# Kernel tuning notes

Hardware: AMD Instinct MI355X
Metric: run time of the kernel (lower is better)

The kernel has to match this reference:

```python
import math
import jax, jax.numpy as jnp
import numpy as np

H = 1024        # hidden_size
V = 32000       # target vocab
T = 64          # decoder steps
B = 32          # batch
NL = 2          # lstm layers
WSZ = 50        # window_size
WLEN = 2 * WSZ + 1
L = 128         # source length (all sequences full)
S = L + WLEN    # padded encoder length, guarantees windows in-bounds
HH = math.ceil(H / 2)
STD2 = (WSZ / 2.0) ** 2
EPS = 1e-14


def setup_inputs():
    key = jax.random.key(0)
    ks = jax.random.split(key, 16)
    sc = 0.02
    inp = {}
    inp["encoder_output"] = jax.random.normal(ks[0], (S, B, H), jnp.float32)
    inp["context"] = jax.random.normal(ks[1], (T, B, H), jnp.float32)
    inp["h0"] = jax.random.normal(ks[2], (NL, B, H), jnp.float32)
    inp["c0"] = jax.random.normal(ks[3], (NL, B, H), jnp.float32)
    inp["embedding"] = jax.random.normal(ks[4], (V, H), jnp.float32) * sc
    inp["attn_w1"] = jax.random.normal(ks[5], (HH, H), jnp.float32) * sc
    inp["attn_b1"] = jnp.zeros((HH,), jnp.float32)
    inp["attn_w2"] = jax.random.normal(ks[6], (1, HH), jnp.float32) * sc
    inp["attn_b2"] = jnp.zeros((1,), jnp.float32)
    inp["lstm_Wih0"] = jax.random.normal(ks[7], (4 * H, 2 * H), jnp.float32) * sc  # input feeding: 2H input
    inp["lstm_Whh0"] = jax.random.normal(ks[8], (4 * H, H), jnp.float32) * sc
    inp["lstm_bih0"] = jnp.zeros((4 * H,), jnp.float32)
    inp["lstm_bhh0"] = jnp.zeros((4 * H,), jnp.float32)
    inp["lstm_Wih1"] = jax.random.normal(ks[9], (4 * H, H), jnp.float32) * sc
    inp["lstm_Whh1"] = jax.random.normal(ks[10], (4 * H, H), jnp.float32) * sc
    inp["lstm_bih1"] = jnp.zeros((4 * H,), jnp.float32)
    inp["lstm_bhh1"] = jnp.zeros((4 * H,), jnp.float32)
    inp["fc1_w"] = jax.random.normal(ks[11], (H, 2 * H), jnp.float32) * sc
    inp["fc1_b"] = jnp.zeros((H,), jnp.float32)
    inp["fc2_w"] = jax.random.normal(ks[12], (V, H), jnp.float32) * sc
    inp["fc2_b"] = jnp.zeros((V,), jnp.float32)
    inp["target_words"] = jax.random.randint(ks[13], (T, B), 0, V)
    inp["lengths"] = jnp.full((B,), L, dtype=jnp.int32)
    return inp


def _lstm_layer(x, h0, c0, Wih, Whh, bih, bhh):
    bias = bih + bhh
    def step(carry, xt):
        h, c = carry
        gates = xt @ Wih.T + h @ Whh.T + bias   # [B, 4H], torch gate order i,f,g,o
        i, f, g, o = jnp.split(gates, 4, axis=-1)
        c = jax.nn.sigmoid(f) * c + jax.nn.sigmoid(i) * jnp.tanh(g)
        h = jax.nn.sigmoid(o) * jnp.tanh(c)
        return (h, c), h
    (hT, cT), ys = jax.lax.scan(step, (h0, c0), x)
    return ys, hT, cT


def _attention(encoder_output, dec_out, lengths, aw1, ab1, aw2, ab2):
    h_s = jnp.transpose(encoder_output, (1, 0, 2))   # [B, S, H]
    h_t = jnp.transpose(dec_out, (1, 0, 2))          # [B, T, H]
    p = jax.nn.sigmoid(jnp.tanh(h_t @ aw1.T + ab1) @ aw2.T + ab2)[..., 0]  # [B, T]
    p = WSZ + lengths[:, None].astype(jnp.float32) * p
    win_start = jnp.round(p - WSZ).astype(jnp.int32)                        # [B, T]
    k = jnp.arange(WLEN)
    positions = win_start[..., None].astype(jnp.float32) + k.astype(jnp.float32)  # [B, T, W]
    gaussian = jnp.exp(-((positions - p[..., None]) ** 2) / (2.0 * STD2))
    # faithful to original: the selection buffer is overwritten every j, so
    # every decoder step attends over the LAST step's window
    sel_idx = win_start[:, -1][:, None] + k                                 # [B, W]
    selection = jnp.take_along_axis(h_s, sel_idx[:, :, None], axis=1)       # [B, W, H]
    score = jnp.einsum('bth,bwh->btw', h_t, selection)
    li = lengths[:, None, None].astype(jnp.int32)
    lo = k[None, None, :] < (WSZ - win_start)[..., None]
    hi = k[None, None, :] >= (li + WSZ - win_start[..., None])
    score = jnp.where(lo | hi, EPS, score)   # original writes epsilon, NOT -inf
    a = jax.nn.softmax(score, axis=2) * gaussian
    c = jnp.einsum('btw,bwh->bth', a, selection)
    return jnp.transpose(c, (1, 0, 2))       # [T, B, H]


def reference(encoder_output, context, h0, c0, embedding,
              attn_w1, attn_b1, attn_w2, attn_b2,
              lstm_Wih0, lstm_Whh0, lstm_bih0, lstm_bhh0,
              lstm_Wih1, lstm_Whh1, lstm_bih1, lstm_bhh1,
              fc1_w, fc1_b, fc2_w, fc2_b,
              target_words, lengths):
    emb = embedding[target_words]                        # [T, B, H]
    x = jnp.concatenate([emb, context], axis=2)          # input feeding -> [T, B, 2H]
    y0, hT0, cT0 = _lstm_layer(x, h0[0], c0[0], lstm_Wih0, lstm_Whh0, lstm_bih0, lstm_bhh0)
    y1, hT1, cT1 = _lstm_layer(y0, h0[1], c0[1], lstm_Wih1, lstm_Whh1, lstm_bih1, lstm_bhh1)
    ctx = _attention(encoder_output, y1, lengths, attn_w1, attn_b1, attn_w2, attn_b2)
    out = jax.nn.relu(jnp.concatenate([ctx, y1], axis=2) @ fc1_w.T + fc1_b)
    y = out @ fc2_w.T + fc2_b                            # [T, B, V]
    h_n = jnp.stack([hT0, hT1])
    c_n = jnp.stack([cT0, cT1])
    return (y, h_n, c_n, ctx)
```

## Files before the change

### kernel.cpp

```cpp
#include <hip/hip_runtime.h>
#include <hip/hip_bf16.h>

#define T_STEPS 64
#define BATCH   32
#define HID     1024
#define VOCAB   32000
#define WLEN_   101
#define WSZ_    50
#define SENC    229
#define LBLK    64

static const size_t Y_SZ   = (size_t)T_STEPS * BATCH * VOCAB;
static const size_t HN_SZ  = (size_t)2 * BATCH * HID;
static const size_t CTX_OFF = Y_SZ + 2 * HN_SZ;

typedef __attribute__((ext_vector_type(8)))  unsigned short us8;
typedef __attribute__((ext_vector_type(8)))  __bf16 bf16x8;
typedef __attribute__((ext_vector_type(4)))  float f32x4;
typedef __attribute__((ext_vector_type(16))) float f32x16;

static __device__ inline unsigned short f2bf(float x) {
    __hip_bfloat16 b = __float2bfloat16(x);
    return __builtin_bit_cast(unsigned short, b);
}

#define GLD_US8_SC(dst, ptr) \
    asm volatile("global_load_dwordx4 %0, %1, off sc0 sc1" : "=v"(dst) : "v"(ptr) : "memory")
#define GLD_F32_SC(dst, ptr) \
    asm volatile("global_load_dword %0, %1, off sc0 sc1" : "=v"(dst) : "v"(ptr) : "memory")
#define GST_U16_SC(ptr, val) \
    asm volatile("global_store_short %0, %1, off sc0 sc1" :: "v"(ptr), "v"(val) : "memory")
#define GST_U32_SC(ptr, val) \
    asm volatile("global_store_dword %0, %1, off sc0 sc1" :: "v"(ptr), "v"(val) : "memory")
#define WAIT_VM0() asm volatile("s_waitcnt vmcnt(0)" ::: "memory")

__global__ __launch_bounds__(256) void gemm_bt(
    const float* __restrict__ A, const float* __restrict__ W,
    const float* __restrict__ b1, const float* __restrict__ b2,
    float* __restrict__ out, int M, int N, int K, int act)
{
    __shared__ __align__(16) float As[16 * 132];
    __shared__ __align__(16) float Ws[16 * 68];
    const int tid  = threadIdx.x;
    const int col0 = blockIdx.x * 64;
    const int row0 = blockIdx.y * 128;
    const int ty   = tid >> 4;
    const int tx   = tid & 15;

    float acc[8][4];
#pragma unroll
    for (int i = 0; i < 8; ++i)
#pragma unroll
        for (int j = 0; j < 4; ++j) acc[i][j] = 0.f;

    for (int k0 = 0; k0 < K; k0 += 16) {
#pragma unroll
        for (int li = 0; li < 2; ++li) {
            int f  = tid + li * 256;
            int r  = f >> 2;
            int kq = (f & 3) << 2;
            float4 v = *reinterpret_cast<const float4*>(A + (size_t)(row0 + r) * K + k0 + kq);
            As[(kq + 0) * 132 + r] = v.x;
            As[(kq + 1) * 132 + r] = v.y;
            As[(kq + 2) * 132 + r] = v.z;
            As[(kq + 3) * 132 + r] = v.w;
        }
        {
            int n  = tid >> 2;
            int kq = (tid & 3) << 2;
            float4 v = *reinterpret_cast<const float4*>(W + (size_t)(col0 + n) * K + k0 + kq);
            Ws[(kq + 0) * 68 + n] = v.x;
            Ws[(kq + 1) * 68 + n] = v.y;
            Ws[(kq + 2) * 68 + n] = v.z;
            Ws[(kq + 3) * 68 + n] = v.w;
        }
        __syncthreads();
#pragma unroll
        for (int k = 0; k < 16; ++k) {
            const float4 a0 = *reinterpret_cast<const float4*>(&As[k * 132 + ty * 8]);
            const float4 a1 = *reinterpret_cast<const float4*>(&As[k * 132 + ty * 8 + 4]);
            const float4 b0 = *reinterpret_cast<const float4*>(&Ws[k * 68 + tx * 4]);
            float av[8] = {a0.x, a0.y, a0.z, a0.w, a1.x, a1.y, a1.z, a1.w};
            float bv[4] = {b0.x, b0.y, b0.z, b0.w};
#pragma unroll
            for (int i = 0; i < 8; ++i)
#pragma unroll
                for (int j = 0; j < 4; ++j) acc[i][j] = fmaf(av[i], bv[j], acc[i][j]);
        }
        __syncthreads();
    }

#pragma unroll
    for (int j = 0; j < 4; ++j) {
        int n = col0 + tx * 4 + j;
        float bias = 0.f;
        if (b1) bias += b1[n];
        if (b2) bias += b2[n];
#pragma unroll
        for (int i = 0; i < 8; ++i) {
            float v = acc[i][j] + bias;
            if (act == 1) v = fmaxf(v, 0.f);
            else if (act == 2) v = tanhf(v);
            out[(size_t)(row0 + ty * 8 + i) * N + n] = v;
        }
    }
}

__global__ __launch_bounds__(256) void gemm_lds_bt(
    const unsigned short* __restrict__ A, const unsigned short* __restrict__ W,
    const float* __restrict__ b1, const float* __restrict__ b2,
    float* __restrict__ out, unsigned short* __restrict__ out_bf,
    int M, int N, int K, int relu)
{
    __shared__ __align__(16) unsigned short As[8192];
    __shared__ __align__(16) unsigned short Ws[8192];
    const int tid  = threadIdx.x;
    const int lane = tid & 63;
    const int wave = tid >> 6;

    const int nwg = gridDim.x;
    const int bid = blockIdx.x;
    const int q = nwg >> 3, r8 = nwg & 7;
    const int xcd = bid & 7, sidx = bid >> 3;
    const int wgid = (xcd < r8 ? xcd * (q + 1) : r8 * (q + 1) + (xcd - r8) * q) + sidx;
    const int mt = M >> 7;
    const int row0 = (wgid % mt) << 7;
    const int col0 = (wgid / mt) << 7;

    const int m0   = (wave >> 1) * 64;
    const int n0   = (wave & 1) * 64;
    const int lrow = lane & 15;
    const int kc   = lane >> 4;

    f32x4 acc[4][4];
#pragma unroll
    for (int i = 0; i < 4; ++i)
#pragma unroll
        for (int j = 0; j < 4; ++j) acc[i][j] = (f32x4){0.f, 0.f, 0.f, 0.f};

    const bool isA = (wave < 2);
    const int  lw  = wave & 1;
    const unsigned short* gbase = isA ? (A + (size_t)row0 * K) : (W + (size_t)col0 * K);
    unsigned short* lbase = isA ? As : Ws;

    for (int k0 = 0; k0 < K; k0 += 64) {
#pragma unroll
        for (int i = 0; i < 8; ++i) {
            const int c    = lw * 512 + i * 64 + lane;
            const int row  = c >> 3;
            const int slot = c & 7;
            const unsigned short* src =
                gbase + (size_t)row * K + k0 + ((slot ^ (row & 7)) << 3);
            __builtin_amdgcn_global_load_lds(
                (const __attribute__((address_space(1))) void*)src,
                (__attribute__((address_space(3))) void*)(lbase + (size_t)(lw * 512 + i * 64) * 8),
                16, 0, 0);
        }
        __syncthreads();
#pragma unroll
        for (int ss = 0; ss < 2; ++ss) {
            us8 a[4], b[4];
#pragma unroll
            for (int f = 0; f < 4; ++f) {
                const int ar = m0 + f * 16 + lrow;
                const int as = (ss * 4 + kc) ^ (ar & 7);
                a[f] = *reinterpret_cast<const us8*>(&As[(ar * 8 + as) * 8]);
                const int br = n0 + f * 16 + lrow;
                const int bs = (ss * 4 + kc) ^ (br & 7);
                b[f] = *reinterpret_cast<const us8*>(&Ws[(br * 8 + bs) * 8]);
            }
#pragma unroll
            for (int fi = 0; fi < 4; ++fi)
#pragma unroll
                for (int fj = 0; fj < 4; ++fj)
                    acc[fi][fj] = __builtin_amdgcn_mfma_f32_16x16x32_bf16(
                        __builtin_bit_cast(bf16x8, a[fi]),
                        __builtin_bit_cast(bf16x8, b[fj]),
                        acc[fi][fj], 0, 0, 0);
        }
        __syncthreads();
    }

#pragma unroll
    for (int fi = 0; fi < 4; ++fi)
#pragma unroll
        for (int fj = 0; fj < 4; ++fj) {
            const int cN = col0 + n0 + fj * 16 + lrow;
            float bv = 0.f;
            if (b1) bv += b1[cN];
            if (b2) bv += b2[cN];
#pragma unroll
            for (int j = 0; j < 4; ++j) {
                const int r = row0 + m0 + fi * 16 + (lane >> 4) * 4 + j;
                float v = acc[fi][fj][j] + bv;
                if (relu) v = fmaxf(v, 0.f);
                if (out)    out[(size_t)r * N + cN] = v;
                if (out_bf) out_bf[(size_t)r * N + cN] = f2bf(v);
            }
        }
}

__global__ void cvt_bf16_kernel(const float* __restrict__ src,
                                unsigned short* __restrict__ dst, int n8)
{
    for (int i = blockIdx.x * blockDim.x + threadIdx.x; i < n8;
         i += gridDim.x * blockDim.x) {
        float4 v0 = *reinterpret_cast<const float4*>(src + (size_t)i * 8);
        float4 v1 = *reinterpret_cast<const float4*>(src + (size_t)i * 8 + 4);
        us8 c = {f2bf(v0.x), f2bf(v0.y), f2bf(v0.z), f2bf(v0.w),
                 f2bf(v1.x), f2bf(v1.y), f2bf(v1.z), f2bf(v1.w)};
        *reinterpret_cast<us8*>(dst + (size_t)i * 8) = c;
    }
}

__global__ void embed_concat_bf_kernel(const float* __restrict__ emb,
                                       const float* __restrict__ ctxin,
                                       const int* __restrict__ tw,
                                       unsigned short* __restrict__ x_bf)
{
    const int total = 2048 * 256;
    for (int idx = blockIdx.x * blockDim.x + threadIdx.x; idx < total;
         idx += gridDim.x * blockDim.x) {
        int row = idx >> 8;
        int c8  = idx & 255;
        const float* src = (c8 < 128)
            ? emb + (size_t)tw[row] * HID + c8 * 8
            : ctxin + (size_t)row * HID + (c8 - 128) * 8;
        float4 v0 = *reinterpret_cast<const float4*>(src);
        float4 v1 = *reinterpret_cast<const float4*>(src + 4);
        us8 c = {f2bf(v0.x), f2bf(v0.y), f2bf(v0.z), f2bf(v0.w),
                 f2bf(v1.x), f2bf(v1.y), f2bf(v1.z), f2bf(v1.w)};
        *reinterpret_cast<us8*>(x_bf + (size_t)idx * 8) = c;
    }
}

__global__ void zero_flags_kernel(int* p, int n)
{
    int i = blockIdx.x * blockDim.x + threadIdx.x;
    if (i < n) p[i] = 0;
}

static __device__ inline void dep_wait(int* __restrict__ flags, int role, int lb,
                                       int q, int tid)
{
    int* epA = flags + 6144;
    int* epC = flags + 6400;
    int* epB = flags + 6656;
    if (lb == 0) {
        if (tid < 64) {
            const int fi = (role * 64 + tid) * 32;
            while (__hip_atomic_load(&flags[fi], __ATOMIC_RELAXED,
                                     __HIP_MEMORY_SCOPE_AGENT) < q + 1)
                __builtin_amdgcn_s_sleep(1);
        }
        __syncthreads();
        int* ep = (role == 0) ? epA : (role == 1 ? epC : epB);
        if (tid < 8)
            __hip_atomic_store(&ep[tid * 32], q + 1,
                               __ATOMIC_RELAXED, __HIP_MEMORY_SCOPE_AGENT);
    }
    int* e1; int t1; int* e2; int t2;
    if (role == 0)      { e1 = epA; t1 = q + 1; e2 = epC; t2 = q - 1; }
    else if (role == 1) { e1 = epA; t1 = q + 1; e2 = epB; t2 = q - 1; }
    else                { e1 = epC; t1 = q + 1; e2 = epB; t2 = q + 1; }
    if (lb == 0) {
        if (role == 0) e1 = nullptr;
        else if (role == 2) e2 = nullptr;
    }
    const int slot = ((int)blockIdx.x & 7) * 32;
    if (tid == 0 && e1) {
        while (__hip_atomic_load(&e1[slot], __ATOMIC_RELAXED,
                                 __HIP_MEMORY_SCOPE_AGENT) < t1)
            __builtin_amdgcn_s_sleep(1);
    }
    if (tid == 64 && e2 && t2 > 1) {
        while (__hip_atomic_load(&e2[slot], __ATOMIC_RELAXED,
                                 __HIP_MEMORY_SCOPE_AGENT) < t2)
            __builtin_amdgcn_s_sleep(1);
    }
    __syncthreads();
}

__global__ __launch_bounds__(256) void lstm_fused3(
    const float* __restrict__ gpre0,
    const float* __restrict__ Whh0, const float* __restrict__ Wih1,
    const float* __restrict__ Whh1,
    const float* __restrict__ bih1, const float* __restrict__ bhh1,
    const float* __restrict__ h0all, const float* __restrict__ c0all,
    float* __restrict__ y1o,
    unsigned short* __restrict__ fin_bf,
    float* __restrict__ hn, float* __restrict__ cn,
    unsigned short* __restrict__ hbf,
    float* __restrict__ part,
    int* __restrict__ flags,
    const float* __restrict__ fc2w, unsigned short* __restrict__ fc2w_bf,
    int foldcvt)
{
    __shared__ __align__(16) us8 WB[8192];
    __shared__ float red2[32 * 132];
    __shared__ float csh[512];

    const int tid  = threadIdx.x;
    const int lane = tid & 63;
    const int w    = tid >> 6;
    const int n    = lane & 31;
    const int kh   = lane >> 5;
    const int bid  = blockIdx.x;
    const int role = bid >> 6;
    const int lb   = bid & 63;
    const int j0   = lb * 16;
    const int b    = tid >> 3;
    const int jj   = tid & 7;

    unsigned short* hb0 = hbf;
    unsigned short* hb1 = hbf + 131072;

    {
        const float* Wsrc = (role == 0) ? Whh0 : (role == 1 ? Wih1 : Whh1);
        const int g = n >> 3, cj = n & 7;
#pragma unroll
        for (int T = 0; T < 2; ++T) {
            const float* wrow = Wsrc + (size_t)(g * HID + j0 + T * 8 + cj) * HID;
#pragma unroll
            for (int f = 0; f < 16; ++f) {
                int k = w * 256 + f * 16 + kh * 8;
                float4 v0 = *reinterpret_cast<const float4*>(wrow + k);
                float4 v1 = *reinterpret_cast<const float4*>(wrow + k + 4);
                WB[((T * 4 + w) * 16 + f) * 64 + lane] =
                    (us8){f2bf(v0.x), f2bf(v0.y), f2bf(v0.z), f2bf(v0.w),
                          f2bf(v1.x), f2bf(v1.y), f2bf(v1.z), f2bf(v1.w)};
            }
        }
    }

    float gp[2][4] = {};
    float bb[2][4] = {};
    if (role == 0) {
#pragma unroll
        for (int T = 0; T < 2; ++T) {
            csh[T * 256 + tid] = c0all[b * HID + j0 + T * 8 + jj];
#pragma unroll
            for (int g = 0; g < 4; ++g)
                gp[T][g] = gpre0[(size_t)b * 4096 + g * HID + j0 + T * 8 + jj];
        }
#pragma unroll
        for (int q = 0; q < 2; ++q) {
            int e = lb * 512 + q * 256 + tid;
            unsigned int hv = f2bf(h0all[((e >> 3) & 31) * HID + (e >> 8) * 8 + (e & 7)]);
            GST_U16_SC(hb0 + e, hv);
        }
    } else if (role == 2) {
#pragma unroll
        for (int T = 0; T < 2; ++T) {
            csh[T * 256 + tid] = c0all[32768 + b * HID + j0 + T * 8 + jj];
#pragma unroll
            for (int g = 0; g < 4; ++g)
                bb[T][g] = bih1[g * HID + j0 + T * 8 + jj] + bhh1[g * HID + j0 + T * 8 + jj];
        }
#pragma unroll
        for (int q = 0; q < 2; ++q) {
            int e = lb * 512 + q * 256 + tid;
            unsigned int hv = f2bf(h0all[32768 + ((e >> 3) & 31) * HID + (e >> 8) * 8 + (e & 7)]);
            GST_U16_SC(hb1 + 32768 + e, hv);
        }
    }

    WAIT_VM0();
    __syncthreads();
    if (tid == 0)
        __hip_atomic_store(&flags[bid * 32], 1, __ATOMIC_RELAXED, __HIP_MEMORY_SCOPE_AGENT);

    for (int p = 0; p <= 65; ++p) {
        dep_wait(flags, role, lb, p, tid);
        const bool active = (role == 0) ? (p <= 63)
                          : (role == 1) ? (p >= 1 && p <= 64)
                                        : (p >= 2);
        if (active) {
            const int t = p - role;
            float pv[2][4];
            if (role == 2) {
                const float* pb = part + (size_t)((p - 2) & 3) * 131072 + lb * 2048 + tid;
#pragma unroll
                for (int T = 0; T < 2; ++T)
#pragma unroll
                    for (int g = 0; g < 4; ++g)
                        GLD_F32_SC(pv[T][g], pb + (T * 4 + g) * 256);
            }
            const unsigned short* hsrc = (role == 2)
                ? hb1 + ((p + 1) & 1) * 32768
                : hb0 + (p & 3) * 32768;
            const unsigned short* hr = hsrc + (size_t)w * 8192 + lane * 8;
            us8 aF[16];
#pragma unroll
            for (int f = 0; f < 16; ++f)
                GLD_US8_SC(aF[f], hr + f * 512);
            WAIT_VM0();
            __builtin_amdgcn_sched_barrier(0);

            f32x16 acc0 = {}, acc1 = {};
#pragma unroll
            for (int f = 0; f < 16; ++f)
                acc0 = __builtin_amdgcn_mfma_f32_32x32x16_bf16(
                    __builtin_bit_cast(bf16x8, aF[f]),
                    __builtin_bit_cast(bf16x8, WB[((0 * 4 + w) * 16 + f) * 64 + lane]),
                    acc0, 0, 0, 0);
#pragma unroll
            for (int f = 0; f < 16; ++f)
                acc1 = __builtin_amdgcn_mfma_f32_32x32x16_bf16(
                    __builtin_bit_cast(bf16x8, aF[f]),
                    __builtin_bit_cast(bf16x8, WB[((1 * 4 + w) * 16 + f) * 64 + lane]),
                    acc1, 0, 0, 0);

#pragma unroll
            for (int T = 0; T < 2; ++T) {
                if (T == 1) __syncthreads();
#pragma unroll
                for (int r = 0; r < 16; ++r) {
                    int m = (r & 3) + 8 * (r >> 2) + 4 * kh;
                    red2[m * 132 + w * 32 + n] = (T == 0) ? acc0[r] : acc1[r];
                }
                __syncthreads();
                float s0, s1, s2, s3;
                {
                    const float* rr = &red2[b * 132 + jj];
                    s0 = rr[0]  + rr[32]  + rr[64]  + rr[96];
                    s1 = rr[8]  + rr[40]  + rr[72]  + rr[104];
                    s2 = rr[16] + rr[48]  + rr[80]  + rr[112];
                    s3 = rr[24] + rr[56]  + rr[88]  + rr[120];
                }
                const int col = j0 + T * 8 + jj;
                const int he  = (lb * 2 + T) * 256 + tid;
                if (role == 1) {
                    float* pdst = part + (size_t)((p - 1) & 3) * 131072 + lb * 2048 + tid;
                    GST_U32_SC(pdst + (T * 4 + 0) * 256, s0);
                    GST_U32_SC(pdst + (T * 4 + 1) * 256, s1);
                    GST_U32_SC(pdst + (T * 4 + 2) * 256, s2);
                    GST_U32_SC(pdst + (T * 4 + 3) * 256, s3);
                } else {
                    if (role == 0) { s0 += gp[T][0]; s1 += gp[T][1]; s2 += gp[T][2]; s3 += gp[T][3]; }
                    else { s0 += pv[T][0] + bb[T][0]; s1 += pv[T][1] + bb[T][1];
                           s2 += pv[T][2] + bb[T][2]; s3 += pv[T][3] + bb[T][3]; }
                    float ig = 1.f / (1.f + expf(-s0));
                    float fg = 1.f / (1.f + expf(-s1));
                    float gg = tanhf(s2);
                    float og = 1.f / (1.f + expf(-s3));
                    float cv = fg * csh[T * 256 + tid] + ig * gg;
                    csh[T * 256 + tid] = cv;
                    float h = og * tanhf(cv);
                    unsigned int hv = f2bf(h);
                    if (role == 0) {
                        GST_U16_SC(hb0 + ((p + 1) & 3) * 32768 + he, hv);
                        if (t == T_STEPS - 1) { hn[b * HID + col] = h; cn[b * HID + col] = cv; }
                    } else {
                        __builtin_nontemporal_store(h, &y1o[(size_t)t * 32768 + b * HID + col]);
                        fin_bf[(size_t)(t * BATCH + b) * 2048 + 1024 + col] = f2bf(h);
                        if (t == T_STEPS - 1) {
                            hn[32768 + b * HID + col] = h;
                            cn[32768 + b * HID + col] = cv;
                        } else {
                            GST_U16_SC(hb1 + (p & 1) * 32768 + he, hv);
                        }
                    }
                }
            }
        }
        if (p < 65) {
            WAIT_VM0();
            __syncthreads();
            if (tid == 0)
                __hip_atomic_store(&flags[bid * 32], p + 2,
                                   __ATOMIC_RELAXED, __HIP_MEMORY_SCOPE_AGENT);
            if (role == 0 && p + 1 <= 63) {
                const float* gsrc = gpre0 + (size_t)((p + 1) * BATCH + b) * 4096 + j0 + jj;
#pragma unroll
                for (int T = 0; T < 2; ++T)
#pragma unroll
                    for (int g = 0; g < 4; ++g)
                        gp[T][g] = gsrc[g * HID + T * 8];
            }
            if (foldcvt && p < 64 && bid >= 64 && bid != 64 && bid != 128) {
                const int cidx = (bid < 128) ? (bid - 65) : (63 + bid - 129);
                const int base = (p * 126 + cidx) * 508;
                for (int j = tid; j < 508; j += 256) {
                    int i = base + j;
                    if (i < 4096000) {
                        float4 v0 = *reinterpret_cast<const float4*>(fc2w + (size_t)i * 8);
                        float4 v1 = *reinterpret_cast<const float4*>(fc2w + (size_t)i * 8 + 4);
                        us8 c = {f2bf(v0.x), f2bf(v0.y), f2bf(v0.z), f2bf(v0.w),
                                 f2bf(v1.x), f2bf(v1.y), f2bf(v1.z), f2bf(v1.w)};
                        *reinterpret_cast<us8*>(fc2w_bf + (size_t)i * 8) = c;
                    }
                }
            }
        }
    }
}

__global__ __launch_bounds__(64) void attn_p_kernel(
    const float* __restrict__ hidden1, const float* __restrict__ aw2,
    const float* __restrict__ ab2, const int* __restrict__ lengths,
    float* __restrict__ p_arr, int* __restrict__ win_arr)
{
    const int row = blockIdx.x;
    const int lane = threadIdx.x;
    float s = 0.f;
    for (int i = lane; i < 512; i += 64) s += hidden1[(size_t)row * 512 + i] * aw2[i];
    for (int off = 32; off > 0; off >>= 1) s += __shfl_down(s, off);
    if (lane == 0) {
        float v = s + ab2[0];
        float sig = 1.f / (1.f + expf(-v));
        int b = row & 31;
        float lf = (float)lengths[b];
        p_arr[row] = (float)WSZ_ + lf * sig;
        win_arr[row] = (int)rintf(lf * sig);
    }
}

__global__ __launch_bounds__(128) void attn_fused_kernel(
    const float* __restrict__ y1, const float* __restrict__ enc,
    const float* __restrict__ p_arr, const int* __restrict__ win_arr,
    const int* __restrict__ lengths, float* __restrict__ ctx,
    unsigned short* __restrict__ fin_bf)
{
    __shared__ __align__(16) float yl[1024];
    __shared__ float sv[WLEN_];
    __shared__ float av[WLEN_];
    const int row = blockIdx.x;
    const int b   = row & 31;
    const int tid = threadIdx.x;

    for (int i = tid; i < 1024; i += 128) yl[i] = y1[(size_t)row * HID + i];
    __syncthreads();

    const int win = win_arr[row];
    const int wl  = win_arr[(T_STEPS - 1) * BATCH + b];
    const float p = p_arr[row];
    const int len = lengths[b];

    if (tid < WLEN_) {
        const float4* s4 = reinterpret_cast<const float4*>(
            enc + ((size_t)(wl + tid) * BATCH + b) * HID);
        const float4* y4 = reinterpret_cast<const float4*>(yl);
        float acc = 0.f;
        for (int q = 0; q < 256; ++q) {
            float4 a = s4[q]; float4 yy = y4[q];
            acc += a.x * yy.x + a.y * yy.y + a.z * yy.z + a.w * yy.w;
        }
        bool lo = tid < (WSZ_ - win);
        bool hi = tid >= (len + WSZ_ - win);
        sv[tid] = (lo || hi) ? 1e-14f : acc;
    }
    __syncthreads();

    float mx = -1e30f;
    for (int w = 0; w < WLEN_; ++w) mx = fmaxf(mx, sv[w]);
    float sum = 0.f;
    for (int w = 0; w < WLEN_; ++w) sum += expf(sv[w] - mx);
    if (tid < WLEN_) {
        float e = expf(sv[tid] - mx) / sum;
        float d = (float)(win + tid) - p;
        av[tid] = e * expf(-(d * d) / 1250.f);
    }
    __syncthreads();

    float acc[8] = {0, 0, 0, 0, 0, 0, 0, 0};
    for (int w = 0; w < WLEN_; ++w) {
        float a = av[w];
        const float* srow = enc + ((size_t)(wl + w) * BATCH + b) * HID;
#pragma unroll
        for (int i = 0; i < 8; ++i) acc[i] += a * srow[tid + 128 * i];
    }
    for (int i = 0; i < 8; ++i) {
        ctx[(size_t)row * HID + tid + 128 * i] = acc[i];
        fin_bf[(size_t)row * 2048 + tid + 128 * i] = f2bf(acc[i]);
    }
}

extern "C" void kernel_launch(void* const* d_in, const int* in_sizes, int n_in,
                              void* d_out, int out_size, void* d_ws, size_t ws_size,
                              hipStream_t stream)
{
    const float* enc   = (const float*)d_in[0];
    const float* ctxin = (const float*)d_in[1];
    const float* h0    = (const float*)d_in[2];
    const float* c0    = (const float*)d_in[3];
    const float* emb   = (const float*)d_in[4];
    const float* aw1   = (const float*)d_in[5];
    const float* ab1   = (const float*)d_in[6];
    const float* aw2   = (const float*)d_in[7];
    const float* ab2   = (const float*)d_in[8];
    const float* Wih0  = (const float*)d_in[9];
    const float* Whh0  = (const float*)d_in[10];
    const float* bih0  = (const float*)d_in[11];
    const float* bhh0  = (const float*)d_in[12];
    const float* Wih1  = (const float*)d_in[13];
    const float* Whh1  = (const float*)d_in[14];
    const float* bih1  = (const float*)d_in[15];
    const float* bhh1  = (const float*)d_in[16];
    const float* fc1w  = (const float*)d_in[17];
    const float* fc1b  = (const float*)d_in[18];
    const float* fc2w  = (const float*)d_in[19];
    const float* fc2b  = (const float*)d_in[20];
    const int*   tw    = (const int*)d_in[21];
    const int*   lens  = (const int*)d_in[22];

    float* ws = (float*)d_ws;
    float*          buf_gates = ws;
    unsigned short* x_bf      = (unsigned short*)(ws + 8388608);
    float*          buf_part  = ws + 8388608;
    unsigned short* Wih0_bf   = (unsigned short*)(ws + 10485760);
    float*          buf_y1    = ws + 16384000;
    unsigned short* buf_hbf   = (unsigned short*)(ws + 18481152);
    int*            buf_flags = (int*)(ws + 18579456);
    float*          buf_hidden1 = ws + 18587904;
    float*          buf_p     = ws + 19636480;
    int*            buf_win   = (int*)(ws + 19638528);
    unsigned short* fin_bf    = (unsigned short*)(ws + 22917376);
    unsigned short* fc1w_bf   = (unsigned short*)(ws + 25014528);
    unsigned short* fc1out_bf = (unsigned short*)(ws + 26063104);

    const size_t fold_end_bytes = (size_t)(27111680 + 8192000) * 4;
    const int foldcvt = (ws_size >= fold_end_bytes) ? 1 : 0;
    unsigned short* fc2w_bf = foldcvt ? (unsigned short*)(ws + 27111680)
                                      : (unsigned short*)ws;

    float* out   = (float*)d_out;
    float* out_hn  = out + Y_SZ;
    float* out_cn  = out + Y_SZ + HN_SZ;
    float* out_ctx = out + CTX_OFF;

    zero_flags_kernel<<<33, 256, 0, stream>>>(buf_flags, 8448);
    cvt_bf16_kernel<<<2048, 256, 0, stream>>>(Wih0, Wih0_bf, 4096 * 2048 / 8);
    cvt_bf16_kernel<<<1024, 256, 0, stream>>>(fc1w, fc1w_bf, 1024 * 2048 / 8);
    embed_concat_bf_kernel<<<2048, 256, 0, stream>>>(emb, ctxin, tw, x_bf);

    gemm_lds_bt<<<512, 256, 0, stream>>>(
        x_bf, Wih0_bf, bih0, bhh0, buf_gates, nullptr, 2048, 4096, 2048, 0);

    lstm_fused3<<<3 * LBLK, 256, 0, stream>>>(
        buf_gates, Whh0, Wih1, Whh1, bih1, bhh1, h0, c0,
        buf_y1, fin_bf, out_hn, out_cn, buf_hbf, buf_part,
        buf_flags, fc2w, fc2w_bf, foldcvt);

    if (!foldcvt)
        cvt_bf16_kernel<<<2048, 256, 0, stream>>>(fc2w, fc2w_bf, VOCAB * HID / 8);

    gemm_bt<<<dim3(512 / 64, 2048 / 128), 256, 0, stream>>>(
        buf_y1, aw1, ab1, nullptr, buf_hidden1, 2048, 512, 1024, 2 );
    attn_p_kernel<<<2048, 64, 0, stream>>>(buf_hidden1, aw2, ab2, lens, buf_p, buf_win);
    attn_fused_kernel<<<2048, 128, 0, stream>>>(buf_y1, enc, buf_p, buf_win, lens,
                                                out_ctx, fin_bf);

    gemm_lds_bt<<<128, 256, 0, stream>>>(
        fin_bf, fc1w_bf, fc1b, nullptr, nullptr, fc1out_bf, 2048, 1024, 2048, 1);

    gemm_lds_bt<<<4000, 256, 0, stream>>>(
        fc1out_bf, fc2w_bf, fc2b, nullptr, out, nullptr, 2048, VOCAB, 1024, 0);
}
```

Measured before the change: 956.1 us.

## Merge prep kernels, replace epoch-based LSTM sync with direct flag polling, nontemporal logits

Four setup kernels (flag zeroing, two weight conversions, embedding gather/concat) are merged into one prep launch to cut launch overhead. The LSTM inter-block dependency wait no longer uses leader-block epoch flags; each block polls all 64 producer flags directly with a wave-wide __all. The folded fc2 weight conversion is redistributed evenly over 128 blocks. The final vocab GEMM writes logits with nontemporal stores to avoid polluting cache. Direct polling adds more atomic traffic, and the flag zeroing range shrinks from 8448 to 6400 entries.

```diff
diff --git a/kernel.cpp b/kernel.cpp
--- a/kernel.cpp
+++ b/kernel.cpp
@@ -110,7 +110,7 @@
     const unsigned short* __restrict__ A, const unsigned short* __restrict__ W,
     const float* __restrict__ b1, const float* __restrict__ b2,
     float* __restrict__ out, unsigned short* __restrict__ out_bf,
-    int M, int N, int K, int relu)
+    int M, int N, int K, int relu, int ntout)
 {
     __shared__ __align__(16) unsigned short As[8192];
     __shared__ __align__(16) unsigned short Ws[8192];
@@ -194,91 +194,69 @@
                 const int r = row0 + m0 + fi * 16 + (lane >> 4) * 4 + j;
                 float v = acc[fi][fj][j] + bv;
                 if (relu) v = fmaxf(v, 0.f);
-                if (out)    out[(size_t)r * N + cN] = v;
+                if (out) {
+                    if (ntout) __builtin_nontemporal_store(v, &out[(size_t)r * N + cN]);
+                    else       out[(size_t)r * N + cN] = v;
+                }
                 if (out_bf) out_bf[(size_t)r * N + cN] = f2bf(v);
             }
         }
 }
 
-__global__ void cvt_bf16_kernel(const float* __restrict__ src,
-                                unsigned short* __restrict__ dst, int n8)
-{
-    for (int i = blockIdx.x * blockDim.x + threadIdx.x; i < n8;
-         i += gridDim.x * blockDim.x) {
-        float4 v0 = *reinterpret_cast<const float4*>(src + (size_t)i * 8);
-        float4 v1 = *reinterpret_cast<const float4*>(src + (size_t)i * 8 + 4);
+__global__ void prep_kernel(const float* __restrict__ Wih0, unsigned short* __restrict__ Wih0_bf,
+                            const float* __restrict__ fc1w, unsigned short* __restrict__ fc1w_bf,
+                            const float* __restrict__ emb, const float* __restrict__ ctxin,
+                            const int* __restrict__ tw, unsigned short* __restrict__ x_bf,
+                            int* __restrict__ flags)
+{
+    const int bid = blockIdx.x, tid = threadIdx.x;
+    if (bid < 2048) {
+#pragma unroll
+        for (int k = 0; k < 2; ++k) {
+            int i = bid * 256 + tid + k * 524288;
+            float4 v0 = *reinterpret_cast<const float4*>(Wih0 + (size_t)i * 8);
+            float4 v1 = *reinterpret_cast<const float4*>(Wih0 + (size_t)i * 8 + 4);
+            us8 c = {f2bf(v0.x), f2bf(v0.y), f2bf(v0.z), f2bf(v0.w),
+                     f2bf(v1.x), f2bf(v1.y), f2bf(v1.z), f2bf(v1.w)};
+            *reinterpret_cast<us8*>(Wih0_bf + (size_t)i * 8) = c;
+        }
+    } else if (bid < 3072) {
+        int i = (bid - 2048) * 256 + tid;
+        float4 v0 = *reinterpret_cast<const float4*>(fc1w + (size_t)i * 8);
+        float4 v1 = *reinterpret_cast<const float4*>(fc1w + (size_t)i * 8 + 4);
         us8 c = {f2bf(v0.x), f2bf(v0.y), f2bf(v0.z), f2bf(v0.w),
                  f2bf(v1.x), f2bf(v1.y), f2bf(v1.z), f2bf(v1.w)};
-        *reinterpret_cast<us8*>(dst + (size_t)i * 8) = c;
-    }
-}
-
-__global__ void embed_concat_bf_kernel(const float* __restrict__ emb,
-                                       const float* __restrict__ ctxin,
-                                       const int* __restrict__ tw,
-                                       unsigned short* __restrict__ x_bf)
-{
-    const int total = 2048 * 256;
-    for (int idx = blockIdx.x * blockDim.x + threadIdx.x; idx < total;
-         idx += gridDim.x * blockDim.x) {
-        int row = idx >> 8;
-        int c8  = idx & 255;
-        const float* src = (c8 < 128)
-            ? emb + (size_t)tw[row] * HID + c8 * 8
-            : ctxin + (size_t)row * HID + (c8 - 128) * 8;
-        float4 v0 = *reinterpret_cast<const float4*>(src);
-        float4 v1 = *reinterpret_cast<const float4*>(src + 4);
-        us8 c = {f2bf(v0.x), f2bf(v0.y), f2bf(v0.z), f2bf(v0.w),
-                 f2bf(v1.x), f2bf(v1.y), f2bf(v1.z), f2bf(v1.w)};
-        *reinterpret_cast<us8*>(x_bf + (size_t)idx * 8) = c;
-    }
-}
-
-__global__ void zero_flags_kernel(int* p, int n)
-{
-    int i = blockIdx.x * blockDim.x + threadIdx.x;
-    if (i < n) p[i] = 0;
-}
-
-static __device__ inline void dep_wait(int* __restrict__ flags, int role, int lb,
-                                       int q, int tid)
-{
-    int* epA = flags + 6144;
-    int* epC = flags + 6400;
-    int* epB = flags + 6656;
-    if (lb == 0) {
-        if (tid < 64) {
-            const int fi = (role * 64 + tid) * 32;
-            while (__hip_atomic_load(&flags[fi], __ATOMIC_RELAXED,
-                                     __HIP_MEMORY_SCOPE_AGENT) < q + 1)
-                __builtin_amdgcn_s_sleep(1);
-        }
-        __syncthreads();
-        int* ep = (role == 0) ? epA : (role == 1 ? epC : epB);
-        if (tid < 8)
-            __hip_atomic_store(&ep[tid * 32], q + 1,
-                               __ATOMIC_RELAXED, __HIP_MEMORY_SCOPE_AGENT);
-    }
-    int* e1; int t1; int* e2; int t2;
-    if (role == 0)      { e1 = epA; t1 = q + 1; e2 = epC; t2 = q - 1; }
-    else if (role == 1) { e1 = epA; t1 = q + 1; e2 = epB; t2 = q - 1; }
-    else                { e1 = epC; t1 = q + 1; e2 = epB; t2 = q + 1; }
-    if (lb == 0) {
-        if (role == 0) e1 = nullptr;
-        else if (role == 2) e2 = nullptr;
-    }
-    const int slot = ((int)blockIdx.x & 7) * 32;
-    if (tid == 0 && e1) {
-        while (__hip_atomic_load(&e1[slot], __ATOMIC_RELAXED,
-                                 __HIP_MEMORY_SCOPE_AGENT) < t1)
-            __builtin_amdgcn_s_sleep(1);
-    }
-    if (tid == 64 && e2 && t2 > 1) {
-        while (__hip_atomic_load(&e2[slot], __ATOMIC_RELAXED,
-                                 __HIP_MEMORY_SCOPE_AGENT) < t2)
-            __builtin_amdgcn_s_sleep(1);
-    }
-    __syncthreads();
+        *reinterpret_cast<us8*>(fc1w_bf + (size_t)i * 8) = c;
+    } else if (bid < 3584) {
+#pragma unroll
+        for (int k = 0; k < 4; ++k) {
+            int idx = (bid - 3072) * 256 + tid + k * 131072;
+            int row = idx >> 8;
+            int c8  = idx & 255;
+            const float* src = (c8 < 128)
+                ? emb + (size_t)tw[row] * HID + c8 * 8
+                : ctxin + (size_t)row * HID + (c8 - 128) * 8;
+            float4 v0 = *reinterpret_cast<const float4*>(src);
+            float4 v1 = *reinterpret_cast<const float4*>(src + 4);
+            us8 c = {f2bf(v0.x), f2bf(v0.y), f2bf(v0.z), f2bf(v0.w),
+                     f2bf(v1.x), f2bf(v1.y), f2bf(v1.z), f2bf(v1.w)};
+            *reinterpret_cast<us8*>(x_bf + (size_t)idx * 8) = c;
+        }
+    } else {
+        for (int i = tid; i < 6400; i += 256) flags[i] = 0;
+    }
+}
+
+static __device__ inline void poll_group(int* __restrict__ flags, int gbase, int target)
+{
+    if (target <= 0) return;
+    const int lane = threadIdx.x & 63;
+    int* fp = &flags[(gbase + lane) * 32];
+    for (;;) {
+        int f = __hip_atomic_load(fp, __ATOMIC_RELAXED, __HIP_MEMORY_SCOPE_AGENT);
+        if (__all(f >= target)) break;
+        __builtin_amdgcn_s_sleep(1);
+    }
 }
 
 __global__ __launch_bounds__(256) void lstm_fused3(
@@ -371,7 +349,15 @@
         __hip_atomic_store(&flags[bid * 32], 1, __ATOMIC_RELAXED, __HIP_MEMORY_SCOPE_AGENT);
 
     for (int p = 0; p <= 65; ++p) {
-        dep_wait(flags, role, lb, p, tid);
+        {
+            int g1, t1, g2, t2;
+            if (role == 0)      { g1 = 0;   t1 = p + 1; g2 = 64;  t2 = p - 1; }
+            else if (role == 1) { g1 = 0;   t1 = p + 1; g2 = 128; t2 = p - 1; }
+            else                { g1 = 64;  t1 = p + 1; g2 = 128; t2 = p + 1; }
+            if (tid < 64)        poll_group(flags, g1, t1);
+            else if (tid < 128)  poll_group(flags, g2, t2);
+            __syncthreads();
+        }
         const bool active = (role == 0) ? (p <= 63)
                           : (role == 1) ? (p >= 1 && p <= 64)
                                         : (p >= 2);
@@ -478,10 +464,10 @@
                     for (int g = 0; g < 4; ++g)
                         gp[T][g] = gsrc[g * HID + T * 8];
             }
-            if (foldcvt && p < 64 && bid >= 64 && bid != 64 && bid != 128) {
-                const int cidx = (bid < 128) ? (bid - 65) : (63 + bid - 129);
-                const int base = (p * 126 + cidx) * 508;
-                for (int j = tid; j < 508; j += 256) {
+            if (foldcvt && p < 64 && bid >= 64) {
+                const int cidx = bid - 64;
+                const int base = (p * 128 + cidx) * 500;
+                for (int j = tid; j < 500; j += 256) {
                     int i = base + j;
                     if (i < 4096000) {
                         float4 v0 = *reinterpret_cast<const float4*>(fc2w + (size_t)i * 8);
@@ -573,6 +559,19 @@
     for (int i = 0; i < 8; ++i) {
         ctx[(size_t)row * HID + tid + 128 * i] = acc[i];
         fin_bf[(size_t)row * 2048 + tid + 128 * i] = f2bf(acc[i]);
+    }
+}
+
+__global__ void cvt_bf16_kernel(const float* __restrict__ src,
+                                unsigned short* __restrict__ dst, int n8)
+{
+    for (int i = blockIdx.x * blockDim.x + threadIdx.x; i < n8;
+         i += gridDim.x * blockDim.x) {
+        float4 v0 = *reinterpret_cast<const float4*>(src + (size_t)i * 8);
+        float4 v1 = *reinterpret_cast<const float4*>(src + (size_t)i * 8 + 4);
+        us8 c = {f2bf(v0.x), f2bf(v0.y), f2bf(v0.z), f2bf(v0.w),
+                 f2bf(v1.x), f2bf(v1.y), f2bf(v1.z), f2bf(v1.w)};
+        *reinterpret_cast<us8*>(dst + (size_t)i * 8) = c;
     }
 }
 
@@ -622,20 +621,20 @@
     const size_t fold_end_bytes = (size_t)(27111680 + 8192000) * 4;
     const int foldcvt = (ws_size >= fold_end_bytes) ? 1 : 0;
     unsigned short* fc2w_bf = foldcvt ? (unsigned short*)(ws + 27111680)
-                                      : (unsigned short*)ws;
+                                      : (unsigned short*)(ws + 8388608);
+
+    if (!foldcvt) fc2w_bf = (unsigned short*)ws;
 
     float* out   = (float*)d_out;
     float* out_hn  = out + Y_SZ;
     float* out_cn  = out + Y_SZ + HN_SZ;
     float* out_ctx = out + CTX_OFF;
 
-    zero_flags_kernel<<<33, 256, 0, stream>>>(buf_flags, 8448);
-    cvt_bf16_kernel<<<2048, 256, 0, stream>>>(Wih0, Wih0_bf, 4096 * 2048 / 8);
-    cvt_bf16_kernel<<<1024, 256, 0, stream>>>(fc1w, fc1w_bf, 1024 * 2048 / 8);
-    embed_concat_bf_kernel<<<2048, 256, 0, stream>>>(emb, ctxin, tw, x_bf);
+    prep_kernel<<<3585, 256, 0, stream>>>(Wih0, Wih0_bf, fc1w, fc1w_bf,
+                                          emb, ctxin, tw, x_bf, buf_flags);
 
     gemm_lds_bt<<<512, 256, 0, stream>>>(
-        x_bf, Wih0_bf, bih0, bhh0, buf_gates, nullptr, 2048, 4096, 2048, 0);
+        x_bf, Wih0_bf, bih0, bhh0, buf_gates, nullptr, 2048, 4096, 2048, 0, 0);
 
     lstm_fused3<<<3 * LBLK, 256, 0, stream>>>(
         buf_gates, Whh0, Wih1, Whh1, bih1, bhh1, h0, c0,
@@ -652,8 +651,8 @@
                                                 out_ctx, fin_bf);
 
     gemm_lds_bt<<<128, 256, 0, stream>>>(
-        fin_bf, fc1w_bf, fc1b, nullptr, nullptr, fc1out_bf, 2048, 1024, 2048, 1);
+        fin_bf, fc1w_bf, fc1b, nullptr, nullptr, fc1out_bf, 2048, 1024, 2048, 1, 0);
 
     gemm_lds_bt<<<4000, 256, 0, stream>>>(
-        fc1out_bf, fc2w_bf, fc2b, nullptr, out, nullptr, 2048, VOCAB, 1024, 0);
-}
+        fc1out_bf, fc2w_bf, fc2b, nullptr, out, nullptr, 2048, VOCAB, 1024, 0, 1);
+}
```

Result: no change. 938.4 us (-1.9%).
